# Kernel tuning notes

Hardware: AMD Instinct MI355X
Metric: run time of the kernel (lower is better)

The kernel has to match this reference:

```python
import jax, jax.numpy as jnp
import numpy as np
import math

B, L, H, U = 4, 4096, 1024, 1024


def setup_inputs() -> dict:
    key = jax.random.key(0)
    k_in, k_wi, k_bi, k_wo, k_bo, k_u = jax.random.split(key, 6)
    inputs = jax.random.normal(k_in, (B, L, H), dtype=jnp.float32)
    # Linear layers (torch Linear: y = x @ W.T + b), scaled like torch default init
    Wi = jax.random.normal(k_wi, (U, H), dtype=jnp.float32) / math.sqrt(H)
    bi = jax.random.normal(k_bi, (U,), dtype=jnp.float32) * 0.01
    Wo = jax.random.normal(k_wo, (H, U), dtype=jnp.float32) / math.sqrt(U)
    bo = jax.random.normal(k_bo, (H,), dtype=jnp.float32) * 0.01
    # LRU-style init of nu_log / gamma_log, exactly as in the torch __init__
    r_min, r_max = 0.9, 0.999
    u = jax.random.uniform(k_u, (U,), dtype=jnp.float32)
    nu_log = jnp.log(-0.5 * jnp.log(u * (r_max ** 2 - r_min ** 2) + r_min ** 2))
    gamma_log = jnp.log(jnp.sqrt(1.0 - jnp.exp(-jnp.exp(nu_log)) ** 2))
    params_log = jnp.stack([nu_log, gamma_log])  # [2, U]
    return {"inputs": inputs, "Wi": Wi, "bi": bi, "Wo": Wo, "bo": bo,
            "params_log": params_log}


def reference(inputs, Wi, bi, Wo, bo, params_log):
    # u = i_dense(inputs): [B, L, U]
    u = jnp.einsum('blh,uh->blu', inputs, Wi) + bi
    params = jnp.exp(params_log)
    nu, gamma = params[0], params[1]  # each [U]

    log2_L = int(np.ceil(np.log2(L)))
    pad_len = 2 ** log2_L - L
    x = jnp.pad(u, ((0, 0), (0, pad_len), (0, 0))) if pad_len else u
    Lp = 2 ** log2_L

    # Log-depth doubling parallel scan: h_t = exp(-nu) * h_{t-1} + u_t
    for i in range(1, log2_L + 1):
        l = 2 ** i
        x = x.reshape(B * Lp // l, l, U)
        x1, x2 = x[:, : l // 2], x[:, l // 2:]
        pos = jnp.arange(1, l // 2 + 1, dtype=jnp.float32)  # [l/2]
        lambs = jnp.exp(-pos[:, None] * nu)                  # [l/2, U]
        x2 = x2 + lambs * x1[:, -1:]
        x = jnp.concatenate([x1, x2], axis=1).reshape(B, Lp, U)

    x = x[:, :L] * gamma
    # o_dense: [B, L, H]
    return jnp.einsum('blu,hu->blh', x, Wo) + bo
```

## Files before the change

kernel.cpp:

```cpp
#include <hip/hip_runtime.h>

#define B_DIM 4
#define L_DIM 4096
#define H_DIM 1024
#define U_DIM 1024
#define M_DIM (B_DIM * L_DIM)
#define LC 64
#define NCH (L_DIM / LC)

using f32x4  = __attribute__((ext_vector_type(4))) float;
using bf16x8 = __attribute__((ext_vector_type(8))) __bf16;
using us8    = __attribute__((ext_vector_type(8))) unsigned short;
using u32x2  = __attribute__((ext_vector_type(2))) unsigned int;

__device__ inline unsigned short f32_to_bf16(float f) {
  unsigned int u = __float_as_uint(f);
  u += 0x7FFF + ((u >> 16) & 1);
  return (unsigned short)(u >> 16);
}
__device__ inline float bf16_to_f32(unsigned short v) {
  return __uint_as_float((unsigned int)v << 16);
}

__device__ inline void async_load16(const void* g, void* l) {
  __builtin_amdgcn_global_load_lds(
      (const __attribute__((address_space(1))) void*)g,
      (__attribute__((address_space(3))) void*)l, 16, 0, 0);
}

#define IN_ELEMS  (M_DIM * H_DIM)
#define WI_ELEMS  (U_DIM * H_DIM)
#define WO_ELEMS  (H_DIM * U_DIM)
#define CVT_TOTAL (IN_ELEMS + WI_ELEMS + WO_ELEMS)

__global__ __launch_bounds__(256) void cvt_all(
    const float* __restrict__ inp, const float* __restrict__ wi,
    const float* __restrict__ wo,
    unsigned short* __restrict__ inp_b, unsigned short* __restrict__ wi_b,
    unsigned short* __restrict__ wo_b)
{
  size_t e = ((size_t)blockIdx.x * 256 + threadIdx.x) * 8;
  if (e >= CVT_TOTAL) return;
  const float* src; unsigned short* dst; size_t off;
  if (e < IN_ELEMS)                 { src = inp; dst = inp_b; off = e; }
  else if (e < IN_ELEMS + WI_ELEMS) { src = wi;  dst = wi_b;  off = e - IN_ELEMS; }
  else                              { src = wo;  dst = wo_b;  off = e - IN_ELEMS - WI_ELEMS; }
  f32x4 a = *(const f32x4*)(src + off);
  f32x4 b = *(const f32x4*)(src + off + 4);
  us8 r;
  r[0] = f32_to_bf16(a.x); r[1] = f32_to_bf16(a.y);
  r[2] = f32_to_bf16(a.z); r[3] = f32_to_bf16(a.w);
  r[4] = f32_to_bf16(b.x); r[5] = f32_to_bf16(b.y);
  r[6] = f32_to_bf16(b.z); r[7] = f32_to_bf16(b.w);
  *(us8*)(dst + off) = r;
}

#define BM 256
#define BN 256
#define BK 64

template <typename OUT>
__global__ __launch_bounds__(512, 2) void gemm256(
    const unsigned short* __restrict__ A, const unsigned short* __restrict__ Bm,
    const float* __restrict__ bias, OUT* __restrict__ C,
    int M, int N, int K)
{
  __shared__ __attribute__((aligned(16))) char lds[131072];

  const int tid  = threadIdx.x;
  const int lane = tid & 63;
  const int wave = tid >> 6;
  const int wm   = wave >> 2;
  const int wn   = wave & 3;

  const int nby = M / BM;
  const int sby = nby >> 3;
  const int p   = blockIdx.x;
  const int xcd = p & 7;
  const int j   = p >> 3;
  const int by  = xcd * sby + (j % sby);
  const int bx  = j / sby;
  const int m0  = by * BM;
  const int n0  = bx * BN;

  const size_t rowb = (size_t)K * 2;
  const int NTk = K / BK;

  const int srow  = tid >> 3;
  const int scs16 = ((tid & 7) ^ (srow & 7)) << 4;
  const char* Ab = (const char*)A;
  const char* Bb = (const char*)Bm;

  auto stA = [&](int buf, int half, int kt) {
    const char* g = Ab + (size_t)(m0 + half * 128 + srow) * rowb + (size_t)kt * 128 + scs16;
    char* d = lds + buf * 65536 + half * 16384 + tid * 16;
    async_load16(g, d);
    async_load16(g + 64 * rowb, d + 8192);
  };
  auto stB = [&](int buf, int half, int kt) {
    const char* g = Bb + (size_t)(n0 + half * 128 + srow) * rowb + (size_t)kt * 128 + scs16;
    char* d = lds + buf * 65536 + 32768 + half * 16384 + tid * 16;
    async_load16(g, d);
    async_load16(g + 64 * rowb, d + 8192);
  };

  const int arow = wm * 128 + (lane & 15);
  const int brow = wn * 64  + (lane & 15);
  const int ch0  = (((lane >> 4)    ) ^ (lane & 7)) << 4;
  const int ch1  = (((lane >> 4) | 4) ^ (lane & 7)) << 4;

  f32x4 acc[8][4];
  #pragma unroll
  for (int i = 0; i < 8; ++i)
    #pragma unroll
    for (int q = 0; q < 4; ++q)
      acc[i][q] = {0.f, 0.f, 0.f, 0.f};

  stA(0, 0, 0); stA(0, 1, 0); stB(0, 0, 0); stB(0, 1, 0);
  stA(1, 0, 1); stA(1, 1, 1);
  asm volatile("s_waitcnt vmcnt(4)" ::: "memory");
  __builtin_amdgcn_sched_barrier(0);
  __builtin_amdgcn_s_barrier();

  for (int w = 0; w < NTk; ++w) {
    const int cur = w & 1;
    const char* pa = lds + cur * 65536 + arow * 128;
    const char* pb = lds + cur * 65536 + 32768 + brow * 128;
    bf16x8 af[8][2], bfr[4][2];

    #pragma unroll
    for (int mi = 0; mi < 4; ++mi) {
      af[mi][0] = *(const bf16x8*)(pa + mi * 2048 + ch0);
      af[mi][1] = *(const bf16x8*)(pa + mi * 2048 + ch1);
    }
    #pragma unroll
    for (int ni = 0; ni < 2; ++ni) {
      bfr[ni][0] = *(const bf16x8*)(pb + ni * 2048 + ch0);
      bfr[ni][1] = *(const bf16x8*)(pb + ni * 2048 + ch1);
    }
    if (w + 1 < NTk) stB(cur ^ 1, 0, w + 1);
    __builtin_amdgcn_s_barrier();
    asm volatile("s_waitcnt lgkmcnt(0)" ::: "memory");
    __builtin_amdgcn_sched_barrier(0);
    __builtin_amdgcn_s_setprio(1);
    #pragma unroll
    for (int mi = 0; mi < 4; ++mi)
      #pragma unroll
      for (int ni = 0; ni < 2; ++ni) {
        acc[mi][ni] = __builtin_amdgcn_mfma_f32_16x16x32_bf16(bfr[ni][0], af[mi][0], acc[mi][ni], 0, 0, 0);
        acc[mi][ni] = __builtin_amdgcn_mfma_f32_16x16x32_bf16(bfr[ni][1], af[mi][1], acc[mi][ni], 0, 0, 0);
      }
    __builtin_amdgcn_s_setprio(0);

    #pragma unroll
    for (int mi = 4; mi < 8; ++mi) {
      af[mi][0] = *(const bf16x8*)(pa + mi * 2048 + ch0);
      af[mi][1] = *(const bf16x8*)(pa + mi * 2048 + ch1);
    }
    if (w + 1 < NTk) stB(cur ^ 1, 1, w + 1);
    __builtin_amdgcn_s_barrier();
    asm volatile("s_waitcnt lgkmcnt(0)" ::: "memory");
    __builtin_amdgcn_sched_barrier(0);
    __builtin_amdgcn_s_setprio(1);
    #pragma unroll
    for (int mi = 4; mi < 8; ++mi)
      #pragma unroll
      for (int ni = 0; ni < 2; ++ni) {
        acc[mi][ni] = __builtin_amdgcn_mfma_f32_16x16x32_bf16(bfr[ni][0], af[mi][0], acc[mi][ni], 0, 0, 0);
        acc[mi][ni] = __builtin_amdgcn_mfma_f32_16x16x32_bf16(bfr[ni][1], af[mi][1], acc[mi][ni], 0, 0, 0);
      }
    __builtin_amdgcn_s_setprio(0);

    #pragma unroll
    for (int ni = 2; ni < 4; ++ni) {
      bfr[ni][0] = *(const bf16x8*)(pb + ni * 2048 + ch0);
      bfr[ni][1] = *(const bf16x8*)(pb + ni * 2048 + ch1);
    }
    __builtin_amdgcn_s_barrier();
    asm volatile("s_waitcnt lgkmcnt(0)" ::: "memory");
    __builtin_amdgcn_sched_barrier(0);
    __builtin_amdgcn_s_setprio(1);
    #pragma unroll
    for (int mi = 0; mi < 4; ++mi)
      #pragma unroll
      for (int ni = 2; ni < 4; ++ni) {
        acc[mi][ni] = __builtin_amdgcn_mfma_f32_16x16x32_bf16(bfr[ni][0], af[mi][0], acc[mi][ni], 0, 0, 0);
        acc[mi][ni] = __builtin_amdgcn_mfma_f32_16x16x32_bf16(bfr[ni][1], af[mi][1], acc[mi][ni], 0, 0, 0);
      }
    __builtin_amdgcn_s_setprio(0);

    if (w + 2 < NTk) { stA(cur, 0, w + 2); stA(cur, 1, w + 2); }
    if (w < NTk - 2) asm volatile("s_waitcnt vmcnt(4)" ::: "memory");
    else             asm volatile("s_waitcnt vmcnt(0)" ::: "memory");
    __builtin_amdgcn_sched_barrier(0);
    __builtin_amdgcn_s_barrier();
    __builtin_amdgcn_s_setprio(1);
    #pragma unroll
    for (int mi = 4; mi < 8; ++mi)
      #pragma unroll
      for (int ni = 2; ni < 4; ++ni) {
        acc[mi][ni] = __builtin_amdgcn_mfma_f32_16x16x32_bf16(bfr[ni][0], af[mi][0], acc[mi][ni], 0, 0, 0);
        acc[mi][ni] = __builtin_amdgcn_mfma_f32_16x16x32_bf16(bfr[ni][1], af[mi][1], acc[mi][ni], 0, 0, 0);
      }
    __builtin_amdgcn_s_setprio(0);
  }

  const int q4 = (lane >> 4) * 4;
  #pragma unroll
  for (int mi = 0; mi < 8; ++mi) {
    const int row = m0 + wm * 128 + mi * 16 + (lane & 15);
    #pragma unroll
    for (int ni = 0; ni < 4; ++ni) {
      const int ncol = n0 + wn * 64 + ni * 16 + q4;
      const f32x4 bv = *(const f32x4*)(bias + ncol);
      f32x4 v = acc[mi][ni];
      v.x += bv.x; v.y += bv.y; v.z += bv.z; v.w += bv.w;
      if constexpr (sizeof(OUT) == 2) {
        u32x2 pk;
        pk.x = ((unsigned)f32_to_bf16(v.y) << 16) | (unsigned)f32_to_bf16(v.x);
        pk.y = ((unsigned)f32_to_bf16(v.w) << 16) | (unsigned)f32_to_bf16(v.z);
        *(u32x2*)((unsigned short*)C + (size_t)row * N + ncol) = pk;
      } else {
        *(f32x4*)((float*)C + (size_t)row * N + ncol) = v;
      }
    }
  }
}

__global__ __launch_bounds__(256) void scan_carry(
    const unsigned short* __restrict__ u, const float* __restrict__ params_log,
    float* __restrict__ carry)
{
  const int u0 = (threadIdx.x & 127) * 8;
  const int c  = blockIdx.x * 2 + (threadIdx.x >> 7);
  const int b  = blockIdx.y;
  f32x4 n0 = *(const f32x4*)(params_log + u0);
  f32x4 n1 = *(const f32x4*)(params_log + u0 + 4);
  float l[8], s[8];
  #pragma unroll
  for (int i = 0; i < 8; ++i) {
    float nv = (i < 4) ? n0[i] : n1[i - 4];
    l[i] = expf(-expf(nv));
    s[i] = 0.f;
  }
  const unsigned short* p = u + (size_t)(b * L_DIM + c * LC) * U_DIM + u0;
  #pragma unroll 8
  for (int j = 0; j < LC; ++j) {
    us8 v = *(const us8*)(p + (size_t)j * U_DIM);
    #pragma unroll
    for (int i = 0; i < 8; ++i)
      s[i] = fmaf(s[i], l[i], bf16_to_f32(v[i]));
  }
  float* cp = carry + ((size_t)b * NCH + c) * U_DIM + u0;
  f32x4 o0 = {s[0], s[1], s[2], s[3]};
  f32x4 o1 = {s[4], s[5], s[6], s[7]};
  *(f32x4*)cp = o0;
  *(f32x4*)(cp + 4) = o1;
}

__global__ __launch_bounds__(256) void scan_papply(
    const unsigned short* __restrict__ u, const float* __restrict__ params_log,
    const float* __restrict__ carry, unsigned short* __restrict__ x_b)
{
  const int u0 = (threadIdx.x & 127) * 8;
  const int c  = blockIdx.x * 2 + (threadIdx.x >> 7);
  const int b  = blockIdx.y;
  f32x4 n0 = *(const f32x4*)(params_log + u0);
  f32x4 n1 = *(const f32x4*)(params_log + u0 + 4);
  f32x4 g0 = *(const f32x4*)(params_log + U_DIM + u0);
  f32x4 g1 = *(const f32x4*)(params_log + U_DIM + u0 + 4);
  float l[8], lp[8], g[8], s[8];
  #pragma unroll
  for (int i = 0; i < 8; ++i) {
    float nv = (i < 4) ? n0[i] : n1[i - 4];
    float e  = expf(nv);
    l[i]  = expf(-e);
    lp[i] = expf(-e * (float)LC);
    g[i]  = expf((i < 4) ? g0[i] : g1[i - 4]);
    s[i]  = 0.f;
  }
  const float* cp = carry + (size_t)b * NCH * U_DIM + u0;
  for (int cc = 0; cc < c; ++cc) {
    f32x4 v0 = *(const f32x4*)(cp + (size_t)cc * U_DIM);
    f32x4 v1 = *(const f32x4*)(cp + (size_t)cc * U_DIM + 4);
    #pragma unroll
    for (int i = 0; i < 8; ++i)
      s[i] = fmaf(s[i], lp[i], (i < 4) ? v0[i] : v1[i - 4]);
  }
  const unsigned short* p = u + (size_t)(b * L_DIM + c * LC) * U_DIM + u0;
  unsigned short* q = x_b + (size_t)(b * L_DIM + c * LC) * U_DIM + u0;
  #pragma unroll 4
  for (int j = 0; j < LC; ++j) {
    us8 v = *(const us8*)(p + (size_t)j * U_DIM);
    us8 o;
    #pragma unroll
    for (int i = 0; i < 8; ++i) {
      s[i] = fmaf(s[i], l[i], bf16_to_f32(v[i]));
      o[i] = f32_to_bf16(s[i] * g[i]);
    }
    *(us8*)(q + (size_t)j * U_DIM) = o;
  }
}

extern "C" void kernel_launch(void* const* d_in, const int* in_sizes, int n_in,
                              void* d_out, int out_size, void* d_ws, size_t ws_size,
                              hipStream_t stream)
{
  const float* inputs     = (const float*)d_in[0];
  const float* Wi         = (const float*)d_in[1];
  const float* bi         = (const float*)d_in[2];
  const float* Wo         = (const float*)d_in[3];
  const float* bo         = (const float*)d_in[4];
  const float* params_log = (const float*)d_in[5];
  float* out = (float*)d_out;

  char* ws = (char*)d_ws;
  unsigned short* u_b    = (unsigned short*)(ws);
  unsigned short* x_b    = (unsigned short*)(ws + (32u << 20));
  unsigned short* in_b   = (unsigned short*)(ws + (64u << 20));
  unsigned short* wi_b   = (unsigned short*)(ws + (96u << 20));
  unsigned short* wo_b   = (unsigned short*)(ws + (98u << 20));
  float*          carry  = (float*)(ws + (100u << 20));

  cvt_all<<<dim3((CVT_TOTAL / 8 + 255) / 256), 256, 0, stream>>>(
      inputs, Wi, Wo, in_b, wi_b, wo_b);

  gemm256<unsigned short><<<dim3((M_DIM / BM) * (U_DIM / BN)), 512, 0, stream>>>(
      in_b, wi_b, bi, u_b, M_DIM, U_DIM, H_DIM);

  scan_carry <<<dim3(NCH / 2, B_DIM), 256, 0, stream>>>(u_b, params_log, carry);
  scan_papply<<<dim3(NCH / 2, B_DIM), 256, 0, stream>>>(u_b, params_log, carry, x_b);

  gemm256<float><<<dim3((M_DIM / BM) * (H_DIM / BN)), 512, 0, stream>>>(
      x_b, wo_b, bo, out, M_DIM, H_DIM, U_DIM);
}
```

Baseline: 238.6 us.

## Replace per-chunk serial carry accumulation with a wavefront parallel prefix scan

Adds a scan_prefix kernel that runs a 64-lane shuffle-based associative scan over the chunk carries, one wavefront per (batch, channel). It writes exclusive prefixes so scan_apply no longer loops serially over all earlier chunks. This removes the O(NCH) serial carry loop in the apply kernel, which made late chunks much slower than early ones. In exchange it adds one extra kernel launch and a prefix buffer round-trip. The scan kernels also move to 128-thread blocks with one chunk per block, giving more, smaller blocks.

```diff
diff --git a/kernel.cpp b/kernel.cpp
--- a/kernel.cpp
+++ b/kernel.cpp
@@ -227,12 +227,12 @@
   }
 }
 
-__global__ __launch_bounds__(256) void scan_carry(
+__global__ __launch_bounds__(128) void scan_carry(
     const unsigned short* __restrict__ u, const float* __restrict__ params_log,
     float* __restrict__ carry)
 {
-  const int u0 = (threadIdx.x & 127) * 8;
-  const int c  = blockIdx.x * 2 + (threadIdx.x >> 7);
+  const int u0 = threadIdx.x * 8;
+  const int c  = blockIdx.x;
   const int b  = blockIdx.y;
   f32x4 n0 = *(const f32x4*)(params_log + u0);
   f32x4 n1 = *(const f32x4*)(params_log + u0 + 4);
@@ -258,38 +258,54 @@
   *(f32x4*)(cp + 4) = o1;
 }
 
-__global__ __launch_bounds__(256) void scan_papply(
+__global__ __launch_bounds__(256) void scan_prefix(
+    const float* __restrict__ carry, const float* __restrict__ params_log,
+    float* __restrict__ prefix)
+{
+  int wid  = (blockIdx.x * 256 + threadIdx.x) >> 6;
+  int lane = threadIdx.x & 63;
+  int b  = wid >> 10;
+  int uu = wid & (U_DIM - 1);
+  float lp = expf(-expf(params_log[uu]) * (float)LC);
+  const float* cp = carry + (size_t)b * NCH * U_DIM + uu;
+  float s = cp[(size_t)lane * U_DIM];
+  float a = lp;
+  #pragma unroll
+  for (int d = 1; d < 64; d <<= 1) {
+    float s_up = __shfl_up(s, d, 64);
+    float a_up = __shfl_up(a, d, 64);
+    if (lane >= d) { s = fmaf(a, s_up, s); a *= a_up; }
+  }
+  float ex = __shfl_up(s, 1, 64);
+  if (lane == 0) ex = 0.f;
+  prefix[((size_t)b * NCH + lane) * U_DIM + uu] = ex;
+}
+
+__global__ __launch_bounds__(128) void scan_apply(
     const unsigned short* __restrict__ u, const float* __restrict__ params_log,
-    const float* __restrict__ carry, unsigned short* __restrict__ x_b)
-{
-  const int u0 = (threadIdx.x & 127) * 8;
-  const int c  = blockIdx.x * 2 + (threadIdx.x >> 7);
+    const float* __restrict__ prefix, unsigned short* __restrict__ x_b)
+{
+  const int u0 = threadIdx.x * 8;
+  const int c  = blockIdx.x;
   const int b  = blockIdx.y;
   f32x4 n0 = *(const f32x4*)(params_log + u0);
   f32x4 n1 = *(const f32x4*)(params_log + u0 + 4);
   f32x4 g0 = *(const f32x4*)(params_log + U_DIM + u0);
   f32x4 g1 = *(const f32x4*)(params_log + U_DIM + u0 + 4);
-  float l[8], lp[8], g[8], s[8];
+  const float* pp = prefix + ((size_t)b * NCH + c) * U_DIM + u0;
+  f32x4 s0 = *(const f32x4*)pp;
+  f32x4 s1 = *(const f32x4*)(pp + 4);
+  float l[8], g[8], s[8];
   #pragma unroll
   for (int i = 0; i < 8; ++i) {
     float nv = (i < 4) ? n0[i] : n1[i - 4];
-    float e  = expf(nv);
-    l[i]  = expf(-e);
-    lp[i] = expf(-e * (float)LC);
-    g[i]  = expf((i < 4) ? g0[i] : g1[i - 4]);
-    s[i]  = 0.f;
-  }
-  const float* cp = carry + (size_t)b * NCH * U_DIM + u0;
-  for (int cc = 0; cc < c; ++cc) {
-    f32x4 v0 = *(const f32x4*)(cp + (size_t)cc * U_DIM);
-    f32x4 v1 = *(const f32x4*)(cp + (size_t)cc * U_DIM + 4);
-    #pragma unroll
-    for (int i = 0; i < 8; ++i)
-      s[i] = fmaf(s[i], lp[i], (i < 4) ? v0[i] : v1[i - 4]);
+    l[i] = expf(-expf(nv));
+    g[i] = expf((i < 4) ? g0[i] : g1[i - 4]);
+    s[i] = (i < 4) ? s0[i] : s1[i - 4];
   }
   const unsigned short* p = u + (size_t)(b * L_DIM + c * LC) * U_DIM + u0;
   unsigned short* q = x_b + (size_t)(b * L_DIM + c * LC) * U_DIM + u0;
-  #pragma unroll 4
+  #pragma unroll 8
   for (int j = 0; j < LC; ++j) {
     us8 v = *(const us8*)(p + (size_t)j * U_DIM);
     us8 o;
@@ -321,6 +337,7 @@
   unsigned short* wi_b   = (unsigned short*)(ws + (96u << 20));
   unsigned short* wo_b   = (unsigned short*)(ws + (98u << 20));
   float*          carry  = (float*)(ws + (100u << 20));
+  float*          prefix = (float*)(ws + (101u << 20));
 
   cvt_all<<<dim3((CVT_TOTAL / 8 + 255) / 256), 256, 0, stream>>>(
       inputs, Wi, Wo, in_b, wi_b, wo_b);
@@ -328,8 +345,9 @@
   gemm256<unsigned short><<<dim3((M_DIM / BM) * (U_DIM / BN)), 512, 0, stream>>>(
       in_b, wi_b, bi, u_b, M_DIM, U_DIM, H_DIM);
 
-  scan_carry <<<dim3(NCH / 2, B_DIM), 256, 0, stream>>>(u_b, params_log, carry);
-  scan_papply<<<dim3(NCH / 2, B_DIM), 256, 0, stream>>>(u_b, params_log, carry, x_b);
+  scan_carry <<<dim3(NCH, B_DIM), 128, 0, stream>>>(u_b, params_log, carry);
+  scan_prefix<<<dim3(B_DIM * U_DIM * 64 / 256), 256, 0, stream>>>(carry, params_log, prefix);
+  scan_apply <<<dim3(NCH, B_DIM), 128, 0, stream>>>(u_b, params_log, prefix, x_b);
 
   gemm256<float><<<dim3((M_DIM / BM) * (H_DIM / BN)), 512, 0, stream>>>(
       x_b, wo_b, bo, out, M_DIM, H_DIM, U_DIM);
```

New measurement: 241.1 us. About the same (+1.0%).
